# Kernel optimization log

Measured on AMD Instinct MI355X. Metric: run time of the kernel, lower is better.

Reference implementation:

```python
import jax, jax.numpy as jnp
import numpy as np

IN_DIM = 1024
OUT_DIM = 1024
NUM_EXPERTS = 8
TOP_K = 2


def setup_inputs() -> dict:
    key = jax.random.key(0)
    ks = jax.random.split(key, 5)
    s = 1.0 / np.sqrt(IN_DIM)
    x = jax.random.normal(ks[0], (4, 2048, IN_DIM), dtype=jnp.float32)
    Wg = jax.random.uniform(ks[1], (IN_DIM, NUM_EXPERTS), jnp.float32, -s, s)
    bg = jnp.zeros((NUM_EXPERTS,), jnp.float32)
    We = jax.random.uniform(ks[2], (NUM_EXPERTS, OUT_DIM, IN_DIM), jnp.float32, -s, s)
    be = jax.random.uniform(ks[3], (NUM_EXPERTS, OUT_DIM), jnp.float32, -s, s)
    return {"x": x, "Wg": Wg, "bg": bg, "We": We, "be": be}


def reference(x, Wg, bg, We, be):
    # gate: softmax over experts
    gate = jax.nn.softmax(x @ Wg + bg, axis=-1)            # [b, s, E]
    # top-k sparsification + renormalization (scatter via one-hot)
    topk_vals, topk_idx = jax.lax.top_k(gate, TOP_K)       # [b, s, K]
    onehot = jax.nn.one_hot(topk_idx, NUM_EXPERTS, dtype=gate.dtype)  # [b,s,K,E]
    gate_sparse = jnp.einsum("bsk,bske->bse", topk_vals, onehot)
    gate_sparse = gate_sparse / jnp.sum(gate_sparse, axis=-1, keepdims=True)
    # dense all-expert compute, then gate-weighted sum (faithful to source)
    y = jnp.einsum("bsi,eoi->bseo", x, We) + be[None, None, :, :].transpose(0, 1, 2, 3)  # [b,s,E,o]
    out = jnp.einsum("bseo,bse->bso", y, gate_sparse)
    return out
```

## Files before the change

### kernel.cpp

```cpp
#include <hip/hip_runtime.h>
#include <hip/hip_bf16.h>

#define TOKENS 8192
#define KDIM 1024
#define NDIM 1024
#define NEXP 8

typedef __attribute__((ext_vector_type(8))) short short8v;
typedef __attribute__((ext_vector_type(8))) unsigned short ushort8v;
typedef __attribute__((ext_vector_type(4))) float f32x4;

__device__ inline unsigned short f2bf(float f) {
  unsigned int u = __float_as_uint(f);
  u += 0x7fffu + ((u >> 16) & 1u);
  return (unsigned short)(u >> 16);
}

__device__ inline void gload_lds16(const void* g, void* l) {
  __builtin_amdgcn_global_load_lds(
      (const __attribute__((address_space(1))) unsigned int*)g,
      (__attribute__((address_space(3))) unsigned int*)l, 16, 0, 0);
}


__global__ __launch_bounds__(256) void gate_conv_kernel(
    const float* __restrict__ x, const float* __restrict__ Wg,
    const float* __restrict__ bg, const float* __restrict__ We,
    unsigned short* __restrict__ xb, unsigned short* __restrict__ Web,
    int* __restrict__ epacked, float2* __restrict__ wpair,
    int* __restrict__ hist, float* __restrict__ out) {
  int b = blockIdx.x;
  int tid = threadIdx.x;
  if (b >= 4352) {
    float4* o = reinterpret_cast<float4*>(out) + (size_t)(b - 4352) * 2048 + tid;
    float4 z = make_float4(0.f, 0.f, 0.f, 0.f);
#pragma unroll
    for (int i = 0; i < 8; ++i) o[i * 256] = z;
    return;
  }
  if (b >= 256) {
    size_t i = (size_t)(b - 256) * 256 + tid;
    const float4* s = reinterpret_cast<const float4*>(We + i * 8);
    float4 a = s[0], c = s[1];
    ushort8v v;
    v[0] = f2bf(a.x); v[1] = f2bf(a.y); v[2] = f2bf(a.z); v[3] = f2bf(a.w);
    v[4] = f2bf(c.x); v[5] = f2bf(c.y); v[6] = f2bf(c.z); v[7] = f2bf(c.w);
    *reinterpret_cast<ushort8v*>(Web + i * 8) = v;
    return;
  }
  __shared__ int lhist[16];
  if (tid < 16) lhist[tid] = 0;
  __syncthreads();
  int w = tid >> 6, lane = tid & 63;
  int tok0 = b * 32 + w * 8;

  for (int t = 0; t < 8; ++t) {
    int tok = tok0 + t;
    const float* xr = x + (size_t)tok * KDIM + lane * 16;
    float acc[NEXP] = {};
    ushort8v xv0, xv1;
#pragma unroll
    for (int j4 = 0; j4 < 4; ++j4) {
      float4 xv = *reinterpret_cast<const float4*>(xr + j4 * 4);
      float xs[4] = {xv.x, xv.y, xv.z, xv.w};
#pragma unroll
      for (int jj = 0; jj < 4; ++jj) {
        int k = lane * 16 + j4 * 4 + jj;
        const float4* wr = reinterpret_cast<const float4*>(Wg + k * NEXP);
        float4 w0 = wr[0], w1 = wr[1];
        float xf = xs[jj];
        acc[0] += xf * w0.x; acc[1] += xf * w0.y;
        acc[2] += xf * w0.z; acc[3] += xf * w0.w;
        acc[4] += xf * w1.x; acc[5] += xf * w1.y;
        acc[6] += xf * w1.z; acc[7] += xf * w1.w;
        int li = j4 * 4 + jj;
        unsigned short bv = f2bf(xf);
        if (li < 8) xv0[li] = bv; else xv1[li - 8] = bv;
      }
    }
    unsigned short* xrow = xb + (size_t)tok * KDIM + lane * 16;
    *reinterpret_cast<ushort8v*>(xrow) = xv0;
    *reinterpret_cast<ushort8v*>(xrow + 8) = xv1;
#pragma unroll
    for (int e = 0; e < NEXP; ++e) {
      acc[e] += __shfl_xor(acc[e], 1, 64);
      acc[e] += __shfl_xor(acc[e], 2, 64);
      acc[e] += __shfl_xor(acc[e], 4, 64);
      acc[e] += __shfl_xor(acc[e], 8, 64);
      acc[e] += __shfl_xor(acc[e], 16, 64);
      acc[e] += __shfl_xor(acc[e], 32, 64);
    }
    if (lane == 0) {
      float lg[NEXP];
#pragma unroll
      for (int e = 0; e < NEXP; ++e) lg[e] = acc[e] + bg[e];
      int e0 = 0;
#pragma unroll
      for (int e = 1; e < NEXP; ++e) if (lg[e] > lg[e0]) e0 = e;
      int e1 = -1;
#pragma unroll
      for (int e = 0; e < NEXP; ++e) {
        if (e == e0) continue;
        if (e1 < 0 || lg[e] > lg[e1]) e1 = e;
      }
      float tv = expf(lg[e1] - lg[e0]);
      float w0 = 1.0f / (1.0f + tv);
      float w1 = tv * w0;
      epacked[tok] = e0 | (e1 << 8);
      wpair[tok] = make_float2(w0, w1);
      atomicAdd(&lhist[e0], 1);
      atomicAdd(&lhist[8 + e1], 1);
    }
  }
  __syncthreads();
  if (tid < 16) hist[b * 16 + tid] = lhist[tid];
}

__global__ __launch_bounds__(256) void scatter_kernel(
    const int* __restrict__ hist, const int* __restrict__ epacked,
    const float2* __restrict__ wpair, int* __restrict__ counts,
    int* __restrict__ lists, float* __restrict__ wlists) {
  __shared__ int partial[16][17];
  __shared__ int base[16];
  __shared__ int cnt2[16];
  int tid = threadIdx.x;
  int b = blockIdx.x;
  int bin = tid & 15, grp = tid >> 4;
  int s = 0;
  for (int i = 0; i < 16; ++i) {
    int bb = grp * 16 + i;
    if (bb < b) s += hist[bb * 16 + bin];
  }
  partial[grp][bin] = s;
  if (tid < 16) cnt2[tid] = 0;
  __syncthreads();
  if (tid < 16) {
    int s2 = 0;
#pragma unroll
    for (int g = 0; g < 16; ++g) s2 += partial[g][tid];
    base[tid] = s2;
  }
  __syncthreads();
  if (tid < 64) {
    int tok = b * 32 + (tid >> 1);
    int slot = tid & 1;
    int ep = epacked[tok];
    int e = slot ? ((ep >> 8) & 255) : (ep & 255);
    float2 wp = wpair[tok];
    float wv = slot ? wp.y : wp.x;
    int bn = slot * 8 + e;
    int pos = base[bn] + atomicAdd(&cnt2[bn], 1);
    lists[bn * TOKENS + pos] = tok;
    wlists[bn * TOKENS + pos] = wv;
  }
  if (b == 255) {
    __syncthreads();
    if (tid < 16) counts[tid] = base[tid] + cnt2[tid];
  }
}

template <int PLAIN>
__global__ __launch_bounds__(512) void moe_gemm_wide(
    const unsigned short* __restrict__ xb, const unsigned short* __restrict__ Web,
    const float* __restrict__ be, const int* __restrict__ counts,
    const int* __restrict__ lists, const float* __restrict__ wlists,
    float* __restrict__ out, float* __restrict__ p1) {
  int id = blockIdx.x;
  int e = id & 7;
  int rest = id >> 3;
  int slot = rest & 1;
  int bx = (rest >> 1) & 3;
  int by = rest >> 3;
  int bz = slot * 8 + e;
  int cnt = counts[bz];
  int mbase = by * 64;
  if (mbase >= cnt) return;
  int nbase = bx * 256;
  const int* lst = lists + bz * TOKENS;
  const float* wl = wlists + bz * TOKENS;

  __shared__ alignas(128) unsigned short lA[64 * 64];
  __shared__ alignas(128) unsigned short lB[256 * 64];

  int tid = threadIdx.x;
  int lane = tid & 63;
  int w = tid >> 6;
  int wm = w >> 2, wn = w & 3;
  int lm = lane & 15, lk = lane >> 4;

  const unsigned short* aga;
  {
    int r = tid >> 3, cs = tid & 7;
    int c = cs ^ (r & 7);
    int gr = mbase + r; if (gr >= cnt) gr = cnt - 1;
    aga = xb + (size_t)lst[gr] * KDIM + c * 8;
  }
  const unsigned short* bga[4];
#pragma unroll
  for (int j = 0; j < 4; ++j) {
    int L = j * 512 + tid;
    int r = L >> 3, cs = L & 7;
    int c = cs ^ (r & 7);
    bga[j] = Web + (size_t)e * (NDIM * KDIM) + (size_t)(nbase + r) * KDIM + c * 8;
  }

#define STAGE(kt)                                                             \
  {                                                                           \
    gload_lds16(aga + (kt) * 64, (char*)lA + w * 1024);                       \
    _Pragma("unroll") for (int j = 0; j < 4; ++j)                             \
      gload_lds16(bga[j] + (kt) * 64, (char*)lB + j * 8192 + w * 1024);       \
  }

  f32x4 acc[2][4] = {};

#define COMPUTE                                                               \
  {                                                                           \
    _Pragma("unroll") for (int ks = 0; ks < 2; ++ks) {                        \
      short8v af[2], bfv[4];                                                  \
      _Pragma("unroll") for (int mi = 0; mi < 2; ++mi) {                      \
        int row = wm * 32 + mi * 16 + lm;                                     \
        int cs = (ks * 4 + lk) ^ (row & 7);                                   \
        af[mi] = *reinterpret_cast<const short8v*>(&lA[row * 64 + cs * 8]);   \
      }                                                                       \
      _Pragma("unroll") for (int nj = 0; nj < 4; ++nj) {                      \
        int row = wn * 64 + nj * 16 + lm;                                     \
        int cs = (ks * 4 + lk) ^ (row & 7);                                   \
        bfv[nj] = *reinterpret_cast<const short8v*>(&lB[row * 64 + cs * 8]);  \
      }                                                                       \
      _Pragma("unroll") for (int mi = 0; mi < 2; ++mi)                        \
        _Pragma("unroll") for (int nj = 0; nj < 4; ++nj)                      \
          acc[mi][nj] = __builtin_amdgcn_mfma_f32_16x16x32_bf16(              \
              af[mi], bfv[nj], acc[mi][nj], 0, 0, 0);                         \
    }                                                                         \
  }

  for (int kt = 0; kt < 16; ++kt) {
    __syncthreads();
    STAGE(kt);
    __syncthreads();
    COMPUTE;
  }
#undef STAGE
#undef COMPUTE

  float* dst = (PLAIN && slot) ? p1 : out;
  float bev[4];
#pragma unroll
  for (int nj = 0; nj < 4; ++nj)
    bev[nj] = be[e * NDIM + nbase + wn * 64 + nj * 16 + lm];
#pragma unroll
  for (int mi = 0; mi < 2; ++mi) {
#pragma unroll
    for (int r = 0; r < 4; ++r) {
      int grow = mbase + wm * 32 + mi * 16 + lk * 4 + r;
      if (grow >= cnt) continue;
      int tokn = lst[grow];
      float wgt = wl[grow];
      float* orow = dst + (size_t)tokn * NDIM + nbase + wn * 64 + lm;
#pragma unroll
      for (int nj = 0; nj < 4; ++nj) {
        float val = wgt * (acc[mi][nj][r] + bev[nj]);
        if (PLAIN) orow[nj * 16] = val;
        else       unsafeAtomicAdd(&orow[nj * 16], val);
      }
    }
  }
}

__global__ __launch_bounds__(256) void combine_kernel(
    float* __restrict__ out, const float* __restrict__ p1) {
  size_t i = (size_t)blockIdx.x * 256 + threadIdx.x;
  float4 a = reinterpret_cast<const float4*>(p1)[i];
  float4 b = reinterpret_cast<float4*>(out)[i];
  b.x += a.x; b.y += a.y; b.z += a.z; b.w += a.w;
  reinterpret_cast<float4*>(out)[i] = b;
}


__global__ __launch_bounds__(256) void gate_kernel(
    const float* __restrict__ x, const float* __restrict__ Wg,
    const float* __restrict__ bg, int* __restrict__ counts,
    int* __restrict__ lists, float* __restrict__ wlists) {
  int gtid = blockIdx.x * blockDim.x + threadIdx.x;
  int tok = gtid >> 6;
  int lane = threadIdx.x & 63;
  if (tok >= TOKENS) return;
  const float* xr = x + (size_t)tok * KDIM + lane * 16;
  float acc[NEXP] = {};
#pragma unroll
  for (int j4 = 0; j4 < 4; ++j4) {
    float4 xv = *reinterpret_cast<const float4*>(xr + j4 * 4);
    float xs[4] = {xv.x, xv.y, xv.z, xv.w};
#pragma unroll
    for (int jj = 0; jj < 4; ++jj) {
      int k = lane * 16 + j4 * 4 + jj;
      const float4* wr = reinterpret_cast<const float4*>(Wg + k * NEXP);
      float4 w0 = wr[0], w1 = wr[1];
      float xv1 = xs[jj];
      acc[0] += xv1 * w0.x; acc[1] += xv1 * w0.y;
      acc[2] += xv1 * w0.z; acc[3] += xv1 * w0.w;
      acc[4] += xv1 * w1.x; acc[5] += xv1 * w1.y;
      acc[6] += xv1 * w1.z; acc[7] += xv1 * w1.w;
    }
  }
#pragma unroll
  for (int e = 0; e < NEXP; ++e) {
    acc[e] += __shfl_xor(acc[e], 1, 64);
    acc[e] += __shfl_xor(acc[e], 2, 64);
    acc[e] += __shfl_xor(acc[e], 4, 64);
    acc[e] += __shfl_xor(acc[e], 8, 64);
    acc[e] += __shfl_xor(acc[e], 16, 64);
    acc[e] += __shfl_xor(acc[e], 32, 64);
  }
  if (lane == 0) {
    float lg[NEXP];
#pragma unroll
    for (int e = 0; e < NEXP; ++e) lg[e] = acc[e] + bg[e];
    int e0 = 0;
#pragma unroll
    for (int e = 1; e < NEXP; ++e) if (lg[e] > lg[e0]) e0 = e;
    int e1 = -1;
#pragma unroll
    for (int e = 0; e < NEXP; ++e) {
      if (e == e0) continue;
      if (e1 < 0 || lg[e] > lg[e1]) e1 = e;
    }
    float t = expf(lg[e1] - lg[e0]);
    float w0 = 1.0f / (1.0f + t);
    float w1 = t * w0;
    int p0 = atomicAdd(&counts[e0], 1);
    lists[e0 * TOKENS + p0] = tok;
    wlists[e0 * TOKENS + p0] = w0;
    int p1 = atomicAdd(&counts[NEXP + e1], 1);
    lists[(NEXP + e1) * TOKENS + p1] = tok;
    wlists[(NEXP + e1) * TOKENS + p1] = w1;
  }
}

template <int ACCUM>
__global__ __launch_bounds__(256) void moe_gemm(
    const float* __restrict__ x, const float* __restrict__ We,
    const float* __restrict__ be, const int* __restrict__ counts,
    const int* __restrict__ lists, const float* __restrict__ wlists,
    float* __restrict__ out, int slot) {
  int e = blockIdx.z;
  int cnt = counts[slot * NEXP + e];
  int mbase = blockIdx.y * 128;
  if (mbase >= cnt) return;
  int nbase = blockIdx.x * 128;
  const int* lst = lists + (slot * NEXP + e) * TOKENS;
  const float* wl = wlists + (slot * NEXP + e) * TOKENS;
  __shared__ ushort8v lA[1024];
  __shared__ ushort8v lB[1024];
  int tid = threadIdx.x;
  int lane = tid & 63;
  int w = tid >> 6;
  int wm = w >> 1, wn = w & 1;
  const float* aptr[4];
  const float* bptr[4];
  int sw[4];
#pragma unroll
  for (int i = 0; i < 4; ++i) {
    int c = i * 256 + tid;
    int r = c >> 3, cc = c & 7;
    int gr = mbase + r;
    if (gr >= cnt) gr = cnt - 1;
    int tokn = lst[gr];
    aptr[i] = x + (size_t)tokn * KDIM + cc * 8;
    bptr[i] = We + (size_t)e * (NDIM * KDIM) + (size_t)(nbase + r) * KDIM + cc * 8;
    sw[i] = r * 8 + (cc ^ (r & 7));
  }
  f32x4 acc[4][4] = {};
  int lm = lane & 15, lk = lane >> 4;
  for (int kt = 0; kt < KDIM / 64; ++kt) {
    __syncthreads();
#pragma unroll
    for (int i = 0; i < 4; ++i) {
      float4 f0 = *reinterpret_cast<const float4*>(aptr[i] + kt * 64);
      float4 f1 = *reinterpret_cast<const float4*>(aptr[i] + kt * 64 + 4);
      ushort8v v;
      v[0] = f2bf(f0.x); v[1] = f2bf(f0.y); v[2] = f2bf(f0.z); v[3] = f2bf(f0.w);
      v[4] = f2bf(f1.x); v[5] = f2bf(f1.y); v[6] = f2bf(f1.z); v[7] = f2bf(f1.w);
      lA[sw[i]] = v;
      float4 g0 = *reinterpret_cast<const float4*>(bptr[i] + kt * 64);
      float4 g1 = *reinterpret_cast<const float4*>(bptr[i] + kt * 64 + 4);
      ushort8v u;
      u[0] = f2bf(g0.x); u[1] = f2bf(g0.y); u[2] = f2bf(g0.z); u[3] = f2bf(g0.w);
      u[4] = f2bf(g1.x); u[5] = f2bf(g1.y); u[6] = f2bf(g1.z); u[7] = f2bf(g1.w);
      lB[sw[i]] = u;
    }
    __syncthreads();
#pragma unroll
    for (int ks = 0; ks < 2; ++ks) {
      short8v af[4], bfv[4];
#pragma unroll
      for (int mi = 0; mi < 4; ++mi) {
        int row = wm * 64 + mi * 16 + lm;
        int cidx = (ks * 4 + lk) ^ (row & 7);
        af[mi] = *reinterpret_cast<const short8v*>(&lA[row * 8 + cidx]);
      }
#pragma unroll
      for (int nj = 0; nj < 4; ++nj) {
        int row = wn * 64 + nj * 16 + lm;
        int cidx = (ks * 4 + lk) ^ (row & 7);
        bfv[nj] = *reinterpret_cast<const short8v*>(&lB[row * 8 + cidx]);
      }
#pragma unroll
      for (int mi = 0; mi < 4; ++mi)
#pragma unroll
        for (int nj = 0; nj < 4; ++nj)
          acc[mi][nj] = __builtin_amdgcn_mfma_f32_16x16x32_bf16(
              af[mi], bfv[nj], acc[mi][nj], 0, 0, 0);
    }
  }
  float bev[4];
#pragma unroll
  for (int nj = 0; nj < 4; ++nj)
    bev[nj] = be[e * NDIM + nbase + wn * 64 + nj * 16 + lm];
#pragma unroll
  for (int mi = 0; mi < 4; ++mi) {
#pragma unroll
    for (int r = 0; r < 4; ++r) {
      int grow = mbase + wm * 64 + mi * 16 + lk * 4 + r;
      if (grow >= cnt) continue;
      int tokn = lst[grow];
      float wgt = wl[grow];
      float* orow = out + (size_t)tokn * NDIM + nbase + wn * 64 + lm;
#pragma unroll
      for (int nj = 0; nj < 4; ++nj) {
        float val = wgt * (acc[mi][nj][r] + bev[nj]);
        if (ACCUM) orow[nj * 16] += val;
        else       orow[nj * 16] = val;
      }
    }
  }
}


extern "C" void kernel_launch(void* const* d_in, const int* in_sizes, int n_in,
                              void* d_out, int out_size, void* d_ws, size_t ws_size,
                              hipStream_t stream) {
  const float* x  = (const float*)d_in[0];
  const float* Wg = (const float*)d_in[1];
  const float* bg = (const float*)d_in[2];
  const float* We = (const float*)d_in[3];
  const float* be = (const float*)d_in[4];
  float* out = (float*)d_out;

  char* p = (char*)d_ws;
  int*   counts = (int*)p;                 p += 256;
  int*   lists  = (int*)p;                 p += (size_t)16 * TOKENS * 4;
  float* wlists = (float*)p;               p += (size_t)16 * TOKENS * 4;
  int*   epacked = (int*)p;                p += (size_t)TOKENS * 4;
  float2* wpair  = (float2*)p;             p += (size_t)TOKENS * 8;
  int*   hist    = (int*)p;                p += 256 * 16 * 4;
  unsigned short* xbuf = (unsigned short*)p; p += (size_t)TOKENS * KDIM * 2;
  unsigned short* Webf = (unsigned short*)p; p += (size_t)NEXP * NDIM * KDIM * 2;
  size_t need_mid = (size_t)(p - (char*)d_ws);
  float* part1 = (float*)p;                p += (size_t)TOKENS * NDIM * 4;
  size_t need_fast = (size_t)(p - (char*)d_ws);

  if (ws_size >= need_fast) {
    gate_conv_kernel<<<4352, 256, 0, stream>>>(
        x, Wg, bg, We, xbuf, Webf, epacked, wpair, hist, out);
    scatter_kernel<<<256, 256, 0, stream>>>(hist, epacked, wpair, counts, lists, wlists);
    moe_gemm_wide<1><<<2048, 512, 0, stream>>>(
        xbuf, Webf, be, counts, lists, wlists, out, part1);
    combine_kernel<<<TOKENS * NDIM / 4 / 256, 256, 0, stream>>>(out, part1);
  } else if (ws_size >= need_mid) {
    gate_conv_kernel<<<5376, 256, 0, stream>>>(
        x, Wg, bg, We, xbuf, Webf, epacked, wpair, hist, out);
    scatter_kernel<<<256, 256, 0, stream>>>(hist, epacked, wpair, counts, lists, wlists);
    moe_gemm_wide<0><<<2048, 512, 0, stream>>>(
        xbuf, Webf, be, counts, lists, wlists, out, out);
  } else {
    dim3 grid(NDIM / 128, TOKENS / 128, NEXP);
    hipMemsetAsync(d_ws, 0, 64, stream);
    gate_kernel<<<TOKENS / 4, 256, 0, stream>>>(x, Wg, bg, counts, lists, wlists);
    moe_gemm<0><<<grid, 256, 0, stream>>>(x, We, be, counts, lists, wlists, out, 0);
    moe_gemm<1><<<grid, 256, 0, stream>>>(x, We, be, counts, lists, wlists, out, 1);
  }
}
```

Baseline: 114.8 us.

## Replace LDS-staged expert GEMM with direct global-to-register MFMA kernel

Adds a moe_gemm_nolds kernel with 256 threads in which each wave loads A and B fragments straight from global memory into registers. It drops the LDS staging and the two barriers per k-step, and each wave now owns a 64x64 output tile. The fast path switches to this kernel. It gives up data reuse through shared memory, so more global/L2 traffic is spent on redundant fragment loads.

```diff
diff --git a/kernel.cpp b/kernel.cpp
--- a/kernel.cpp
+++ b/kernel.cpp
@@ -160,7 +160,7 @@
 }
 
 template <int PLAIN>
-__global__ __launch_bounds__(512) void moe_gemm_wide(
+__global__ __launch_bounds__(256) void moe_gemm_nolds(
     const unsigned short* __restrict__ xb, const unsigned short* __restrict__ Web,
     const float* __restrict__ be, const int* __restrict__ counts,
     const int* __restrict__ lists, const float* __restrict__ wlists,
@@ -179,15 +179,100 @@
   const int* lst = lists + bz * TOKENS;
   const float* wl = wlists + bz * TOKENS;
 
+  int lane = threadIdx.x & 63;
+  int w = threadIdx.x >> 6;
+  int lm = lane & 15, lk = lane >> 4;
+
+  const unsigned short* arow[4];
+#pragma unroll
+  for (int mi = 0; mi < 4; ++mi) {
+    int gr = mbase + mi * 16 + lm;
+    if (gr >= cnt) gr = cnt - 1;
+    arow[mi] = xb + (size_t)lst[gr] * KDIM + lk * 8;
+  }
+  const unsigned short* brow[4];
+#pragma unroll
+  for (int nj = 0; nj < 4; ++nj)
+    brow[nj] = Web + (size_t)e * (NDIM * KDIM) +
+               (size_t)(nbase + w * 64 + nj * 16 + lm) * KDIM + lk * 8;
+
+  f32x4 acc[4][4] = {};
+#pragma unroll 4
+  for (int kt = 0; kt < 32; ++kt) {
+    short8v af[4], bfv[4];
+#pragma unroll
+    for (int mi = 0; mi < 4; ++mi)
+      af[mi] = *reinterpret_cast<const short8v*>(arow[mi] + kt * 32);
+#pragma unroll
+    for (int nj = 0; nj < 4; ++nj)
+      bfv[nj] = *reinterpret_cast<const short8v*>(brow[nj] + kt * 32);
+#pragma unroll
+    for (int mi = 0; mi < 4; ++mi)
+#pragma unroll
+      for (int nj = 0; nj < 4; ++nj)
+        acc[mi][nj] = __builtin_amdgcn_mfma_f32_16x16x32_bf16(
+            af[mi], bfv[nj], acc[mi][nj], 0, 0, 0);
+  }
+
+  float* dst = (PLAIN && slot) ? p1 : out;
+  float bev[4];
+#pragma unroll
+  for (int nj = 0; nj < 4; ++nj)
+    bev[nj] = be[e * NDIM + nbase + w * 64 + nj * 16 + lm];
+#pragma unroll
+  for (int mi = 0; mi < 4; ++mi) {
+#pragma unroll
+    for (int r = 0; r < 4; ++r) {
+      int grow = mbase + mi * 16 + lk * 4 + r;
+      if (grow >= cnt) continue;
+      int tokn = lst[grow];
+      float wgt = wl[grow];
+      float* orow = dst + (size_t)tokn * NDIM + nbase + w * 64 + lm;
+#pragma unroll
+      for (int nj = 0; nj < 4; ++nj) {
+        float val = wgt * (acc[mi][nj][r] + bev[nj]);
+        if (PLAIN) orow[nj * 16] = val;
+        else       unsafeAtomicAdd(&orow[nj * 16], val);
+      }
+    }
+  }
+}
+
+__global__ __launch_bounds__(256) void combine_kernel(
+    float* __restrict__ out, const float* __restrict__ p1) {
+  size_t i = (size_t)blockIdx.x * 256 + threadIdx.x;
+  float4 a = reinterpret_cast<const float4*>(p1)[i];
+  float4 b = reinterpret_cast<float4*>(out)[i];
+  b.x += a.x; b.y += a.y; b.z += a.z; b.w += a.w;
+  reinterpret_cast<float4*>(out)[i] = b;
+}
+
+
+__global__ __launch_bounds__(512) void moe_gemm_wide(
+    const unsigned short* __restrict__ xb, const unsigned short* __restrict__ Web,
+    const float* __restrict__ be, const int* __restrict__ counts,
+    const int* __restrict__ lists, const float* __restrict__ wlists,
+    float* __restrict__ out) {
+  int id = blockIdx.x;
+  int e = id & 7;
+  int rest = id >> 3;
+  int slot = rest & 1;
+  int bx = (rest >> 1) & 3;
+  int by = rest >> 3;
+  int bz = slot * 8 + e;
+  int cnt = counts[bz];
+  int mbase = by * 64;
+  if (mbase >= cnt) return;
+  int nbase = bx * 256;
+  const int* lst = lists + bz * TOKENS;
+  const float* wl = wlists + bz * TOKENS;
   __shared__ alignas(128) unsigned short lA[64 * 64];
   __shared__ alignas(128) unsigned short lB[256 * 64];
-
   int tid = threadIdx.x;
   int lane = tid & 63;
   int w = tid >> 6;
   int wm = w >> 2, wn = w & 3;
   int lm = lane & 15, lk = lane >> 4;
-
   const unsigned short* aga;
   {
     int r = tid >> 3, cs = tid & 7;
@@ -203,16 +288,13 @@
     int c = cs ^ (r & 7);
     bga[j] = Web + (size_t)e * (NDIM * KDIM) + (size_t)(nbase + r) * KDIM + c * 8;
   }
-
 #define STAGE(kt)                                                             \
   {                                                                           \
     gload_lds16(aga + (kt) * 64, (char*)lA + w * 1024);                       \
     _Pragma("unroll") for (int j = 0; j < 4; ++j)                             \
       gload_lds16(bga[j] + (kt) * 64, (char*)lB + j * 8192 + w * 1024);       \
   }
-
   f32x4 acc[2][4] = {};
-
 #define COMPUTE                                                               \
   {                                                                           \
     _Pragma("unroll") for (int ks = 0; ks < 2; ++ks) {                        \
@@ -233,7 +315,6 @@
               af[mi], bfv[nj], acc[mi][nj], 0, 0, 0);                         \
     }                                                                         \
   }
-
   for (int kt = 0; kt < 16; ++kt) {
     __syncthreads();
     STAGE(kt);
@@ -242,8 +323,6 @@
   }
 #undef STAGE
 #undef COMPUTE
-
-  float* dst = (PLAIN && slot) ? p1 : out;
   float bev[4];
 #pragma unroll
   for (int nj = 0; nj < 4; ++nj)
@@ -256,24 +335,12 @@
       if (grow >= cnt) continue;
       int tokn = lst[grow];
       float wgt = wl[grow];
-      float* orow = dst + (size_t)tokn * NDIM + nbase + wn * 64 + lm;
-#pragma unroll
-      for (int nj = 0; nj < 4; ++nj) {
-        float val = wgt * (acc[mi][nj][r] + bev[nj]);
-        if (PLAIN) orow[nj * 16] = val;
-        else       unsafeAtomicAdd(&orow[nj * 16], val);
-      }
-    }
-  }
-}
-
-__global__ __launch_bounds__(256) void combine_kernel(
-    float* __restrict__ out, const float* __restrict__ p1) {
-  size_t i = (size_t)blockIdx.x * 256 + threadIdx.x;
-  float4 a = reinterpret_cast<const float4*>(p1)[i];
-  float4 b = reinterpret_cast<float4*>(out)[i];
-  b.x += a.x; b.y += a.y; b.z += a.z; b.w += a.w;
-  reinterpret_cast<float4*>(out)[i] = b;
+      float* orow = out + (size_t)tokn * NDIM + nbase + wn * 64 + lm;
+#pragma unroll
+      for (int nj = 0; nj < 4; ++nj)
+        unsafeAtomicAdd(&orow[nj * 16], wgt * (acc[mi][nj][r] + bev[nj]));
+    }
+  }
 }
 
 
@@ -464,15 +531,15 @@
     gate_conv_kernel<<<4352, 256, 0, stream>>>(
         x, Wg, bg, We, xbuf, Webf, epacked, wpair, hist, out);
     scatter_kernel<<<256, 256, 0, stream>>>(hist, epacked, wpair, counts, lists, wlists);
-    moe_gemm_wide<1><<<2048, 512, 0, stream>>>(
+    moe_gemm_nolds<1><<<2048, 256, 0, stream>>>(
         xbuf, Webf, be, counts, lists, wlists, out, part1);
     combine_kernel<<<TOKENS * NDIM / 4 / 256, 256, 0, stream>>>(out, part1);
   } else if (ws_size >= need_mid) {
     gate_conv_kernel<<<5376, 256, 0, stream>>>(
         x, Wg, bg, We, xbuf, Webf, epacked, wpair, hist, out);
     scatter_kernel<<<256, 256, 0, stream>>>(hist, epacked, wpair, counts, lists, wlists);
-    moe_gemm_wide<0><<<2048, 512, 0, stream>>>(
-        xbuf, Webf, be, counts, lists, wlists, out, out);
+    moe_gemm_wide<<<2048, 512, 0, stream>>>(
+        xbuf, Webf, be, counts, lists, wlists, out);
   } else {
     dim3 grid(NDIM / 128, TOKENS / 128, NEXP);
     hipMemsetAsync(d_ws, 0, 64, stream);
```

New measurement: 212.6 us. 1.85x slower.

## Split MoE GEMM into two sequential slot passes, dropping partial buffer and combine

Applied to the files above, without the earlier changes.

The old path ran one GEMM launch that wrote the first top-k slot into the output and the second slot into a separate partial buffer, then ran a combine kernel to sum them. The new path launches the GEMM twice. The first launch stores slot-0 results directly and the second does a read-modify-write add for slot 1, so the 32MB partial buffer, the combine pass and the output-zeroing blocks all go away. In exchange, each launch has half the blocks, which may leave fewer blocks to fill the GPU, and the second pass serialises behind the first.

```diff
diff --git a/kernel.cpp b/kernel.cpp
--- a/kernel.cpp
+++ b/kernel.cpp
@@ -28,16 +28,9 @@
     const float* __restrict__ bg, const float* __restrict__ We,
     unsigned short* __restrict__ xb, unsigned short* __restrict__ Web,
     int* __restrict__ epacked, float2* __restrict__ wpair,
-    int* __restrict__ hist, float* __restrict__ out) {
+    int* __restrict__ hist) {
   int b = blockIdx.x;
   int tid = threadIdx.x;
-  if (b >= 4352) {
-    float4* o = reinterpret_cast<float4*>(out) + (size_t)(b - 4352) * 2048 + tid;
-    float4 z = make_float4(0.f, 0.f, 0.f, 0.f);
-#pragma unroll
-    for (int i = 0; i < 8; ++i) o[i * 256] = z;
-    return;
-  }
   if (b >= 256) {
     size_t i = (size_t)(b - 256) * 256 + tid;
     const float4* s = reinterpret_cast<const float4*>(We + i * 8);
@@ -159,19 +152,18 @@
   }
 }
 
-template <int PLAIN>
+template <int MODE>
 __global__ __launch_bounds__(512) void moe_gemm_wide(
     const unsigned short* __restrict__ xb, const unsigned short* __restrict__ Web,
     const float* __restrict__ be, const int* __restrict__ counts,
     const int* __restrict__ lists, const float* __restrict__ wlists,
-    float* __restrict__ out, float* __restrict__ p1) {
+    float* __restrict__ out) {
   int id = blockIdx.x;
   int e = id & 7;
   int rest = id >> 3;
-  int slot = rest & 1;
-  int bx = (rest >> 1) & 3;
-  int by = rest >> 3;
-  int bz = slot * 8 + e;
+  int bx = rest & 3;
+  int by = rest >> 2;
+  int bz = MODE * 8 + e;
   int cnt = counts[bz];
   int mbase = by * 64;
   if (mbase >= cnt) return;
@@ -243,7 +235,6 @@
 #undef STAGE
 #undef COMPUTE
 
-  float* dst = (PLAIN && slot) ? p1 : out;
   float bev[4];
 #pragma unroll
   for (int nj = 0; nj < 4; ++nj)
@@ -256,24 +247,15 @@
       if (grow >= cnt) continue;
       int tokn = lst[grow];
       float wgt = wl[grow];
-      float* orow = dst + (size_t)tokn * NDIM + nbase + wn * 64 + lm;
+      float* orow = out + (size_t)tokn * NDIM + nbase + wn * 64 + lm;
 #pragma unroll
       for (int nj = 0; nj < 4; ++nj) {
         float val = wgt * (acc[mi][nj][r] + bev[nj]);
-        if (PLAIN) orow[nj * 16] = val;
-        else       unsafeAtomicAdd(&orow[nj * 16], val);
-      }
-    }
-  }
-}
-
-__global__ __launch_bounds__(256) void combine_kernel(
-    float* __restrict__ out, const float* __restrict__ p1) {
-  size_t i = (size_t)blockIdx.x * 256 + threadIdx.x;
-  float4 a = reinterpret_cast<const float4*>(p1)[i];
-  float4 b = reinterpret_cast<float4*>(out)[i];
-  b.x += a.x; b.y += a.y; b.z += a.z; b.w += a.w;
-  reinterpret_cast<float4*>(out)[i] = b;
+        if (MODE == 0) orow[nj * 16] = val;
+        else           orow[nj * 16] += val;
+      }
+    }
+  }
 }
 
 
@@ -456,23 +438,16 @@
   int*   hist    = (int*)p;                p += 256 * 16 * 4;
   unsigned short* xbuf = (unsigned short*)p; p += (size_t)TOKENS * KDIM * 2;
   unsigned short* Webf = (unsigned short*)p; p += (size_t)NEXP * NDIM * KDIM * 2;
-  size_t need_mid = (size_t)(p - (char*)d_ws);
-  float* part1 = (float*)p;                p += (size_t)TOKENS * NDIM * 4;
-  size_t need_fast = (size_t)(p - (char*)d_ws);
-
-  if (ws_size >= need_fast) {
+  size_t need = (size_t)(p - (char*)d_ws);
+
+  if (ws_size >= need) {
     gate_conv_kernel<<<4352, 256, 0, stream>>>(
-        x, Wg, bg, We, xbuf, Webf, epacked, wpair, hist, out);
+        x, Wg, bg, We, xbuf, Webf, epacked, wpair, hist);
     scatter_kernel<<<256, 256, 0, stream>>>(hist, epacked, wpair, counts, lists, wlists);
-    moe_gemm_wide<1><<<2048, 512, 0, stream>>>(
-        xbuf, Webf, be, counts, lists, wlists, out, part1);
-    combine_kernel<<<TOKENS * NDIM / 4 / 256, 256, 0, stream>>>(out, part1);
-  } else if (ws_size >= need_mid) {
-    gate_conv_kernel<<<5376, 256, 0, stream>>>(
-        x, Wg, bg, We, xbuf, Webf, epacked, wpair, hist, out);
-    scatter_kernel<<<256, 256, 0, stream>>>(hist, epacked, wpair, counts, lists, wlists);
-    moe_gemm_wide<0><<<2048, 512, 0, stream>>>(
-        xbuf, Webf, be, counts, lists, wlists, out, out);
+    moe_gemm_wide<0><<<1024, 512, 0, stream>>>(
+        xbuf, Webf, be, counts, lists, wlists, out);
+    moe_gemm_wide<1><<<1024, 512, 0, stream>>>(
+        xbuf, Webf, be, counts, lists, wlists, out);
   } else {
     dim3 grid(NDIM / 128, TOKENS / 128, NEXP);
     hipMemsetAsync(d_ws, 0, 64, stream);
```

New measurement: 124.0 us. 8.0% more time.
